# Performance work log

Hardware: AMD Instinct MI355X
Metric: run time of the kernel (lower is better)

## Reference

```python
import jax, jax.numpy as jnp
import numpy as np
import math

HIST = 10  # attention window over per-node prediction history


def setup_inputs() -> dict:
    key = jax.random.key(0)
    ks = jax.random.split(key, 16)
    N, DEG, F, H, M, O, P, S = 512, 8, 128, 256, 256, 64, 2, 64

    def lin(k, fan_in, shape):
        b = 1.0 / np.sqrt(fan_in)
        return jax.random.uniform(k, shape, jnp.float32, -b, b)

    return {
        "xa": jax.random.normal(ks[0], (N, F), jnp.float32),
        "neighbors": jax.random.randint(ks[1], (N, DEG), 0, N),
        "first_message": jax.random.normal(ks[2], (N, M), jnp.float32),
        "We": lin(ks[3], F, (F, H)), "be": lin(ks[3], F, (H,)),
        "Wq": lin(ks[4], M, (M, H)), "bq": lin(ks[4], M, (H,)),
        "Wk": lin(ks[5], H, (H, H)), "bk": lin(ks[5], H, (H,)),
        "Wr": lin(ks[6], 4 * H, (4 * H, H)), "br": lin(ks[6], 4 * H, (H,)),
        "Wm": lin(ks[7], H + M, (H + M, M)), "bm": lin(ks[7], H + M, (M,)),
        "Wd": lin(ks[8], H, (P, H, O)), "bd": lin(ks[8], H, (P, O)),
        "num_starts": S,
    }


def reference(xa, neighbors, first_message, We, be, Wq, bq, Wk, bk,
              Wr, br, Wm, bm, Wd, bd, num_starts):
    N, H = xa.shape[0], We.shape[1]
    M = first_message.shape[1]
    DEG = neighbors.shape[1]
    max_steps = 10 * N                    # message budget, as in the while-loop cap
    CAP = num_starts + max_steps * DEG    # static queue capacity bound
    inv_sqrt_h = 1.0 / math.sqrt(H)
    nbrs = neighbors.astype(jnp.int32)
    slot_ids = jnp.arange(HIST)

    encoded = xa @ We + be                                    # [N,H]
    hist = jnp.zeros((N, HIST, H), xa.dtype).at[:, 0, :].set(encoded)
    count = jnp.ones((N,), jnp.int32)
    q_node = jnp.zeros((CAP,), jnp.int32).at[:num_starts].set(
        jnp.arange(num_starts, dtype=jnp.int32))
    q_msg = jnp.zeros((CAP, M), xa.dtype).at[:num_starts].set(
        first_message[:num_starts])
    head = jnp.int32(0)
    tail = jnp.int32(num_starts)

    def step(carry, _):
        hist, count, q_node, q_msg, head, tail = carry
        active = head < tail                 # queue non-empty
        node = q_node[head]
        message = q_msg[head]                # [M]
        feats = hist[node]                   # [HIST,H] ring buffer of last states
        c = count[node]
        valid = slot_ids < jnp.minimum(c, HIST)
        # NOTE: source uses queries[0]/keys[0] for every head -> heads identical
        query = message @ Wq + bq            # [H]
        keys = feats @ Wk + bk               # [HIST,H]
        logits = jnp.where(valid, keys @ query * inv_sqrt_h, -jnp.inf)
        attn = jax.nn.softmax(logits)        # softmax over history axis (dim=-0)
        values = attn @ feats                # [H]
        newstate = jnp.concatenate([values] * 4) @ Wr + br     # [H]
        newmessage = jnp.concatenate([newstate, message]) @ Wm + bm  # [M]
        # conditional state updates (no-op writes when inactive)
        slot = c % HIST
        hist = hist.at[node, slot].set(jnp.where(active, newstate, hist[node, slot]))
        count = count.at[node].add(jnp.where(active, 1, 0))
        old_n = jax.lax.dynamic_slice(q_node, (tail,), (DEG,))
        old_m = jax.lax.dynamic_slice(q_msg, (tail, 0), (DEG, M))
        q_node = jax.lax.dynamic_update_slice(
            q_node, jnp.where(active, nbrs[node], old_n), (tail,))
        q_msg = jax.lax.dynamic_update_slice(
            q_msg, jnp.where(active, jnp.broadcast_to(newmessage, (DEG, M)), old_m),
            (tail, 0))
        head = head + jnp.where(active, 1, 0)
        tail = tail + jnp.where(active, DEG, 0)
        return (hist, count, q_node, q_msg, head, tail), None

    (hist, count, _, _, _, _), _ = jax.lax.scan(
        step, (hist, count, q_node, q_msg, head, tail), None, length=max_steps)

    final = hist[jnp.arange(N), (count - 1) % HIST]           # [N,H] last state
    logits = jnp.einsum('nh,pho->pno', final, Wd) + bd[:, None, :]
    return jax.nn.log_softmax(logits, axis=-1)                # [P,N,O]
```

## Files before the change

### kernel.cpp

```cpp
#include <hip/hip_runtime.h>
#include <hip/hip_bf16.h>

#define NN 512
#define DEG 8
#define FD 128
#define HD 256
#define MD 256
#define OD 64
#define PD 2
#define HIST 10
#define TOTAL (10 * NN)
#define NPAR 648
#define INV_SQRT_H 0.0625f

typedef __hip_bfloat16 bf16;

__device__ __forceinline__ float finz(float x) {
  unsigned u = __float_as_uint(x);
  return (((u >> 23) & 0xFFu) == 0xFFu) ? 0.f : x;
}

__device__ __forceinline__ float ldin(const void* p, int idx, int bf) {
  if (bf) return __bfloat162float(((const bf16*)p)[idx]);
  return ((const float*)p)[idx];
}

__device__ __forceinline__ float scload(const float* p) {
  return __uint_as_float(__hip_atomic_load((const unsigned*)p, __ATOMIC_RELAXED,
                                           __HIP_MEMORY_SCOPE_AGENT));
}
__device__ __forceinline__ void scstore(float* p, float v) {
  __hip_atomic_store((unsigned*)p, __float_as_uint(v), __ATOMIC_RELAXED,
                     __HIP_MEMORY_SCOPE_AGENT);
}

__device__ float g_hist[NN * HIST * HD];
__device__ float g_msgb[NPAR * MD];
__device__ float g_WQK[HD * HD];
__device__ float g_WrS[HD * HD];
__device__ float g_vq[HD];
__device__ float g_ck[HD];
__device__ float g_bqk;
__device__ int   g_node[TOTAL];
__device__ int   g_rank[TOTAL];
__device__ int   g_counts[NN];
__device__ int   g_off[NN];
__device__ int   g_list[TOTAL];
__device__ int   g_done[TOTAL];
__device__ int   g_dtype;
__device__ int   g_i64;

__device__ __forceinline__ int decode_S(const int* dS) {
  int r = dS[0];
  if (r >= 1 && r <= NN) return r;
  float f = __int_as_float(r);
  if (f >= 1.f && f <= (float)NN) return (int)f;
  unsigned u = ((unsigned)r & 0xFFFFu) << 16;
  float g = __uint_as_float(u);
  if (g >= 1.f && g <= (float)NN) return (int)g;
  return 64;
}

__device__ __forceinline__ int get_nbr(const int* nbrs, int i64, int n, int d) {
  int v = i64 ? nbrs[2 * (n * DEG + d)] : nbrs[n * DEG + d];
  return (v < 0) ? 0 : (v >= NN ? NN - 1 : v);
}

__global__ void __launch_bounds__(1024)
k_bfs(const unsigned* __restrict__ xa_w, const int* __restrict__ nbrs,
      const int* __restrict__ dS) {
  __shared__ int s_node[TOTAL];
  __shared__ int s_flags[1];
  const int t = threadIdx.x;
  if (t == 0) {
    int cnt = 0;
    for (int w = 0; w < 64; ++w) {
      unsigned lo = xa_w[w] & 0xFFFFu;
      float av = fabsf(__uint_as_float(lo << 16));
      if (av > 0.000244140625f && av < 64.f) ++cnt;
    }
    g_dtype = (cnt >= 32) ? 1 : 0;
    int allz = 1;
    for (int w = 1; w < 16; w += 2) allz &= (nbrs[w] == 0);
    g_i64 = allz;
    s_flags[0] = allz;
  }
  __syncthreads();
  const int i64 = s_flags[0];
  const int S = decode_S(dS);
  for (int i = t; i < S; i += 1024) s_node[i] = i;
  __syncthreads();
  int done = S;
  while (done < TOTAL) {
    long long nd = (long long)S + 8LL * (long long)done;
    int new_done = nd > (long long)TOTAL ? TOTAL : (int)nd;
    for (int i = done + t; i < new_done; i += 1024)
      s_node[i] = get_nbr(nbrs, i64, s_node[(i - S) >> 3], (i - S) & 7);
    __syncthreads();
    done = new_done;
  }
  for (int i = t; i < TOTAL; i += 1024) g_node[i] = s_node[i];
}

__global__ void __launch_bounds__(64)
k_rank() {
  const int n = blockIdx.x;
  const int l = threadIdx.x;
  if (l < HIST) g_done[n * HIST + l] = 0;
  int k = 0;
  for (int base = 0; base < TOTAL; base += 64) {
    int nd = g_node[base + l];
    unsigned long long m = __ballot(nd == n);
    if (nd == n) {
      unsigned long long below = m & ((1ull << l) - 1ull);
      g_rank[base + l] = k + (int)__popcll(below);
    }
    k += (int)__popcll(m);
  }
  if (l == 0) g_counts[n] = k;
}

__global__ void __launch_bounds__(1024)
k_csr() {
  __shared__ int s_sc[NN];
  const int t = threadIdx.x;
  if (t < NN) s_sc[t] = g_counts[t];
  __syncthreads();
  for (int d = 1; d < NN; d <<= 1) {
    int v = 0;
    if (t < NN && t >= d) v = s_sc[t - d];
    __syncthreads();
    if (t < NN) s_sc[t] += v;
    __syncthreads();
  }
  if (t < NN) g_off[t] = s_sc[t] - g_counts[t];
  __syncthreads();
  for (int e = t; e < TOTAL; e += 1024) {
    const int n = g_node[e];
    g_list[(s_sc[n] - g_counts[n]) + g_rank[e]] = e;
  }
}

__global__ void __launch_bounds__(1024)
k_weights(const void* __restrict__ xa, const void* __restrict__ We,
          const void* __restrict__ be, const void* __restrict__ Wq,
          const void* __restrict__ Wk, const void* __restrict__ Wr,
          const void* __restrict__ bq, const void* __restrict__ bk) {
  const int b = blockIdx.x, t = threadIdx.x;
  const int col = t & 255, grp = t >> 8;
  const int wave = t >> 6, lane = t & 63;
  const int bf = g_dtype;
  __shared__ float sw[HD];
  __shared__ float sp[4][HD];
  __shared__ float sr[16];
  if (b < HD) {
    if (grp == 0) sw[col] = ldin(Wq, b * HD + col, bf);
    __syncthreads();
    {
      const int h0 = grp * 64;
      float a0 = 0.f, a1 = 0.f, a2 = 0.f, a3 = 0.f;
      for (int h = 0; h < 64; h += 4) {
        a0 += sw[h0 + h]     * ldin(Wk, col * HD + h0 + h,     bf);
        a1 += sw[h0 + h + 1] * ldin(Wk, col * HD + h0 + h + 1, bf);
        a2 += sw[h0 + h + 2] * ldin(Wk, col * HD + h0 + h + 2, bf);
        a3 += sw[h0 + h + 3] * ldin(Wk, col * HD + h0 + h + 3, bf);
      }
      sp[grp][col] = (a0 + a1) + (a2 + a3);
    }
    if (grp == 1) {
      float pv = sw[col] * ldin(bk, col, bf);
#pragma unroll
      for (int off = 32; off > 0; off >>= 1) pv += __shfl_down(pv, off, 64);
      if (lane == 0) sr[wave] = pv;
    }
    if (grp == 2) {
      float s = 0.f;
#pragma unroll
      for (int q = 0; q < 4; ++q) s += ldin(Wr, (size_t)(q * HD + b) * HD + col, bf);
      g_WrS[b * HD + col] = s;
    }
    __syncthreads();
    if (grp == 0)
      g_WQK[b * HD + col] = (sp[0][col] + sp[1][col]) + (sp[2][col] + sp[3][col]);
    if (t == 0) g_vq[b] = (sr[4] + sr[5]) + (sr[6] + sr[7]);
  } else if (b == HD) {
    {
      const int h0 = grp * 64;
      float a0 = 0.f, a1 = 0.f, a2 = 0.f, a3 = 0.f;
      for (int h = 0; h < 64; h += 4) {
        a0 += ldin(Wk, col * HD + h0 + h,     bf) * ldin(bq, h0 + h,     bf);
        a1 += ldin(Wk, col * HD + h0 + h + 1, bf) * ldin(bq, h0 + h + 1, bf);
        a2 += ldin(Wk, col * HD + h0 + h + 2, bf) * ldin(bq, h0 + h + 2, bf);
        a3 += ldin(Wk, col * HD + h0 + h + 3, bf) * ldin(bq, h0 + h + 3, bf);
      }
      sp[grp][col] = (a0 + a1) + (a2 + a3);
    }
    if (grp == 1) {
      float pb = ldin(bq, col, bf) * ldin(bk, col, bf);
#pragma unroll
      for (int off = 32; off > 0; off >>= 1) pb += __shfl_down(pb, off, 64);
      if (lane == 0) sr[wave] = pb;
    }
    __syncthreads();
    if (grp == 0)
      g_ck[col] = (sp[0][col] + sp[1][col]) + (sp[2][col] + sp[3][col]);
    if (t == 0) g_bqk = (sr[4] + sr[5]) + (sr[6] + sr[7]);
  } else {
    const int n = b - HD - 1;
    if (t < FD) sw[t] = ldin(xa, n * FD + t, bf);
    __syncthreads();
    const int f0 = grp * 32;
    float a0 = 0.f, a1 = 0.f, a2 = 0.f, a3 = 0.f;
    for (int f = 0; f < 32; f += 4) {
      a0 += sw[f0 + f]     * ldin(We, (f0 + f)     * HD + col, bf);
      a1 += sw[f0 + f + 1] * ldin(We, (f0 + f + 1) * HD + col, bf);
      a2 += sw[f0 + f + 2] * ldin(We, (f0 + f + 2) * HD + col, bf);
      a3 += sw[f0 + f + 3] * ldin(We, (f0 + f + 3) * HD + col, bf);
    }
    sp[grp][col] = (a0 + a1) + (a2 + a3);
    __syncthreads();
    if (grp == 0)
      g_hist[(size_t)(n * HIST) * HD + col] =
          ldin(be, col, bf) + (sp[0][col] + sp[1][col]) + (sp[2][col] + sp[3][col]);
  }
}

__global__ void __launch_bounds__(256, 2)
k_flow(const void* __restrict__ fmsg, const void* __restrict__ br_,
       const void* __restrict__ Wm, const void* __restrict__ bm,
       const int* __restrict__ dS) {
  const int n = blockIdx.x;
  const int t = threadIdx.x;
  const int wave = t >> 6, lane = t & 63;
  const int S = decode_S(dS);
  const int bf = g_dtype;
  __shared__ float s_hist[HIST][HD];
  __shared__ float s_msg[MD];
  __shared__ float s_vals[HD];
  __shared__ float s_ns[HD];
  __shared__ float s_red[4][HIST + 1];
  const int cnt = g_counts[n];
  const int off = g_off[n];
#pragma unroll
  for (int j = 1; j < HIST; ++j) s_hist[j][t] = 0.f;
  s_hist[0][t] = finz(g_hist[(size_t)n * HIST * HD + t]);
  __syncthreads();

  for (int k = 0; k < cnt; ++k) {
    const int e = g_list[off + k];
    const int c = k + 1;
    const int v = (c < HIST) ? c : HIST;
    const int slot = c % HIST;
    const bool hc = (S + 8 * e) < TOTAL;

    float ms;
    if (e < S) {
      ms = ldin(fmsg, e * MD + t, bf);
    } else {
      const int p = (e - S) >> 3;
      if (t == 0)
        while (__hip_atomic_load(&g_done[p], __ATOMIC_RELAXED,
                                 __HIP_MEMORY_SCOPE_AGENT) == 0)
          __builtin_amdgcn_s_sleep(4);
      __syncthreads();
      ms = scload(g_msgb + (size_t)p * MD + t);
    }
    s_msg[t] = finz(ms);
    __syncthreads();

    float a0 = 0.f, a1 = 0.f, a2 = 0.f, a3 = 0.f;
    for (int m = 0; m < MD; m += 4) {
      a0 += s_msg[m]     * g_WQK[(m)     * HD + t];
      a1 += s_msg[m + 1] * g_WQK[(m + 1) * HD + t];
      a2 += s_msg[m + 2] * g_WQK[(m + 2) * HD + t];
      a3 += s_msg[m + 3] * g_WQK[(m + 3) * HD + t];
    }
    const float kq = g_ck[t] + ((a0 + a1) + (a2 + a3));

    float part[HIST + 1];
#pragma unroll
    for (int j = 0; j < HIST; ++j) part[j] = s_hist[j][t] * kq;
    part[HIST] = s_msg[t] * g_vq[t];
#pragma unroll
    for (int o = 32; o > 0; o >>= 1) {
#pragma unroll
      for (int j = 0; j <= HIST; ++j) part[j] += __shfl_down(part[j], o, 64);
    }
    if (lane == 0) {
#pragma unroll
      for (int j = 0; j <= HIST; ++j) s_red[wave][j] = part[j];
    }
    __syncthreads();

    float sc[HIST + 1];
#pragma unroll
    for (int j = 0; j <= HIST; ++j)
      sc[j] = (s_red[0][j] + s_red[1][j]) + (s_red[2][j] + s_red[3][j]);
    const float bkq = sc[HIST] + g_bqk;
    float lg[HIST];
#pragma unroll
    for (int j = 0; j < HIST; ++j)
      lg[j] = (j < v) ? ((sc[j] + bkq) * INV_SQRT_H) : -1e30f;
    float mx = lg[0];
#pragma unroll
    for (int j = 1; j < HIST; ++j) mx = fmaxf(mx, lg[j]);
    float e_[HIST], den = 0.f;
#pragma unroll
    for (int j = 0; j < HIST; ++j) { e_[j] = __expf(lg[j] - mx); den += e_[j]; }
    const float iden = 1.0f / den;
    float val = 0.f;
#pragma unroll
    for (int j = 0; j < HIST; ++j) val += e_[j] * s_hist[j][t];
    s_vals[t] = val * iden;
    __syncthreads();

    float b0 = 0.f, b1 = 0.f, b2 = 0.f, b3 = 0.f;
    for (int h = 0; h < HD; h += 4) {
      b0 += s_vals[h]     * g_WrS[(h)     * HD + t];
      b1 += s_vals[h + 1] * g_WrS[(h + 1) * HD + t];
      b2 += s_vals[h + 2] * g_WrS[(h + 2) * HD + t];
      b3 += s_vals[h + 3] * g_WrS[(h + 3) * HD + t];
    }
    const float ns = ldin(br_, t, bf) + ((b0 + b1) + (b2 + b3));
    s_hist[slot][t] = ns;
    if (k == cnt - 1)
      g_hist[(size_t)(n * HIST + slot) * HD + t] = ns;
    if (hc) s_ns[t] = ns;
    __syncthreads();

    if (hc) {
      float c0 = 0.f, c1 = 0.f, c2 = 0.f, c3 = 0.f;
      if (bf) {
        const bf16* w = (const bf16*)Wm;
        for (int h = 0; h < HD; h += 4) {
          c0 += s_ns[h]     * __bfloat162float(w[(h)     * MD + t]);
          c1 += s_ns[h + 1] * __bfloat162float(w[(h + 1) * MD + t]);
          c2 += s_ns[h + 2] * __bfloat162float(w[(h + 2) * MD + t]);
          c3 += s_ns[h + 3] * __bfloat162float(w[(h + 3) * MD + t]);
        }
        for (int m = 0; m < MD; m += 4) {
          c0 += s_msg[m]     * __bfloat162float(w[(HD + m)     * MD + t]);
          c1 += s_msg[m + 1] * __bfloat162float(w[(HD + m + 1) * MD + t]);
          c2 += s_msg[m + 2] * __bfloat162float(w[(HD + m + 2) * MD + t]);
          c3 += s_msg[m + 3] * __bfloat162float(w[(HD + m + 3) * MD + t]);
        }
      } else {
        const float* w = (const float*)Wm;
        for (int h = 0; h < HD; h += 4) {
          c0 += s_ns[h]     * w[(h)     * MD + t];
          c1 += s_ns[h + 1] * w[(h + 1) * MD + t];
          c2 += s_ns[h + 2] * w[(h + 2) * MD + t];
          c3 += s_ns[h + 3] * w[(h + 3) * MD + t];
        }
        for (int m = 0; m < MD; m += 4) {
          c0 += s_msg[m]     * w[(HD + m)     * MD + t];
          c1 += s_msg[m + 1] * w[(HD + m + 1) * MD + t];
          c2 += s_msg[m + 2] * w[(HD + m + 2) * MD + t];
          c3 += s_msg[m + 3] * w[(HD + m + 3) * MD + t];
        }
      }
      scstore(&g_msgb[(size_t)e * MD + t],
              ldin(bm, t, bf) + ((c0 + c1) + (c2 + c3)));
      asm volatile("s_waitcnt vmcnt(0)" ::: "memory");
    }
    __syncthreads();
    if (hc && t == 0)
      __hip_atomic_store(&g_done[e], 1, __ATOMIC_RELAXED,
                         __HIP_MEMORY_SCOPE_AGENT);
  }
}

__global__ void k_out(const void* __restrict__ Wd, const void* __restrict__ bd,
                      void* __restrict__ out) {
  __shared__ float sf[HD];
  const int b = blockIdx.x;
  const int pp = b >> 9;
  const int n = b & 511;
  const int t = threadIdx.x;
  const int bf = g_dtype;
  int occ = g_counts[n];
  if (occ < 0 || occ > TOTAL) occ = 0;
  const int slot = occ % HIST;
  for (int h = t; h < HD; h += OD) sf[h] = finz(g_hist[(size_t)(n * HIST + slot) * HD + h]);
  __syncthreads();
  float acc = finz(ldin(bd, pp * OD + t, bf));
  for (int h = 0; h < HD; ++h) acc += sf[h] * ldin(Wd, (pp * HD + h) * OD + t, bf);
  acc = finz(acc);
  float mx = acc;
#pragma unroll
  for (int off = 32; off > 0; off >>= 1) mx = fmaxf(mx, __shfl_xor(mx, off, 64));
  float ex = __expf(acc - mx);
  float s = ex;
#pragma unroll
  for (int off = 32; off > 0; off >>= 1) s += __shfl_xor(s, off, 64);
  float r = finz(acc - mx - logf(s));
  const int oi = (pp * NN + n) * OD + t;
  if (bf) ((bf16*)out)[oi] = __float2bfloat16(r);
  else    ((float*)out)[oi] = r;
}

extern "C" void kernel_launch(void* const* d_in, const int* in_sizes, int n_in,
                              void* d_out, int out_size, void* d_ws, size_t ws_size,
                              hipStream_t stream) {
  const void* xa   = d_in[0];
  const int*  nbrs = (const int*)d_in[1];
  const void* fmsg = d_in[2];
  const void* We   = d_in[3];
  const void* be   = d_in[4];
  const void* Wq   = d_in[5];
  const void* bq   = d_in[6];
  const void* Wk   = d_in[7];
  const void* bk   = d_in[8];
  const void* Wr   = d_in[9];
  const void* br   = d_in[10];
  const void* Wm   = d_in[11];
  const void* bm   = d_in[12];
  const void* Wd   = d_in[13];
  const void* bd   = d_in[14];
  const int*  dS   = (const int*)d_in[15];
  (void)d_ws; (void)ws_size; (void)in_sizes; (void)n_in; (void)out_size;

  k_bfs<<<dim3(1), dim3(1024), 0, stream>>>((const unsigned*)xa, nbrs, dS);
  k_rank<<<dim3(NN), dim3(64), 0, stream>>>();
  k_csr<<<dim3(1), dim3(1024), 0, stream>>>();
  k_weights<<<dim3(HD + 1 + NN), dim3(1024), 0, stream>>>(xa, We, be, Wq, Wk, Wr, bq, bk);
  k_flow<<<dim3(NN), dim3(256), 0, stream>>>(fmsg, br, Wm, bm, dS);
  k_out<<<dim3(PD * NN), dim3(OD), 0, stream>>>(Wd, bd, d_out);
}
```

Measured before the change: 482.4 us.

## Fuse prep kernels, build per-node lists in flow, and split matvecs across waves

Merges the BFS, rank, CSR and weight-precompute launches into one prep kernel. Each flow block now builds its own list of queue entries by scanning g_node in shared memory, so the global rank/CSR passes go away. The per-step matvecs (WQK, WrS, Wm) are split across the four waves by reduction dimension, with float4/ushort4 column loads and a shared-memory reduce. The attention score reduction now covers only three values per wave instead of eleven. In exchange each serial step gets more barriers, and the 20KB s_list plus the 20KB s_node array in the prep kernel raise shared-memory use, which may reduce occupancy.

```diff
diff --git a/kernel.cpp b/kernel.cpp
--- a/kernel.cpp
+++ b/kernel.cpp
@@ -25,6 +25,10 @@
   return ((const float*)p)[idx];
 }
 
+__device__ __forceinline__ float bfu(unsigned short u) {
+  return __uint_as_float(((unsigned)u) << 16);
+}
+
 __device__ __forceinline__ float scload(const float* p) {
   return __uint_as_float(__hip_atomic_load((const unsigned*)p, __ATOMIC_RELAXED,
                                            __HIP_MEMORY_SCOPE_AGENT));
@@ -42,10 +46,7 @@
 __device__ float g_ck[HD];
 __device__ float g_bqk;
 __device__ int   g_node[TOTAL];
-__device__ int   g_rank[TOTAL];
 __device__ int   g_counts[NN];
-__device__ int   g_off[NN];
-__device__ int   g_list[TOTAL];
 __device__ int   g_done[TOTAL];
 __device__ int   g_dtype;
 __device__ int   g_i64;
@@ -66,93 +67,30 @@
   return (v < 0) ? 0 : (v >= NN ? NN - 1 : v);
 }
 
+__device__ __forceinline__ int detect_bf(const unsigned* xa_w) {
+  const int lane = threadIdx.x & 63;
+  unsigned lo = xa_w[lane] & 0xFFFFu;
+  float av = fabsf(__uint_as_float(lo << 16));
+  unsigned long long m = __ballot(av > 0.000244140625f && av < 64.f);
+  return ((int)__popcll(m) >= 32) ? 1 : 0;
+}
+
 __global__ void __launch_bounds__(1024)
-k_bfs(const unsigned* __restrict__ xa_w, const int* __restrict__ nbrs,
-      const int* __restrict__ dS) {
-  __shared__ int s_node[TOTAL];
-  __shared__ int s_flags[1];
-  const int t = threadIdx.x;
-  if (t == 0) {
-    int cnt = 0;
-    for (int w = 0; w < 64; ++w) {
-      unsigned lo = xa_w[w] & 0xFFFFu;
-      float av = fabsf(__uint_as_float(lo << 16));
-      if (av > 0.000244140625f && av < 64.f) ++cnt;
-    }
-    g_dtype = (cnt >= 32) ? 1 : 0;
-    int allz = 1;
-    for (int w = 1; w < 16; w += 2) allz &= (nbrs[w] == 0);
-    g_i64 = allz;
-    s_flags[0] = allz;
-  }
-  __syncthreads();
-  const int i64 = s_flags[0];
-  const int S = decode_S(dS);
-  for (int i = t; i < S; i += 1024) s_node[i] = i;
-  __syncthreads();
-  int done = S;
-  while (done < TOTAL) {
-    long long nd = (long long)S + 8LL * (long long)done;
-    int new_done = nd > (long long)TOTAL ? TOTAL : (int)nd;
-    for (int i = done + t; i < new_done; i += 1024)
-      s_node[i] = get_nbr(nbrs, i64, s_node[(i - S) >> 3], (i - S) & 7);
-    __syncthreads();
-    done = new_done;
-  }
-  for (int i = t; i < TOTAL; i += 1024) g_node[i] = s_node[i];
-}
-
-__global__ void __launch_bounds__(64)
-k_rank() {
-  const int n = blockIdx.x;
-  const int l = threadIdx.x;
-  if (l < HIST) g_done[n * HIST + l] = 0;
-  int k = 0;
-  for (int base = 0; base < TOTAL; base += 64) {
-    int nd = g_node[base + l];
-    unsigned long long m = __ballot(nd == n);
-    if (nd == n) {
-      unsigned long long below = m & ((1ull << l) - 1ull);
-      g_rank[base + l] = k + (int)__popcll(below);
-    }
-    k += (int)__popcll(m);
-  }
-  if (l == 0) g_counts[n] = k;
-}
-
-__global__ void __launch_bounds__(1024)
-k_csr() {
-  __shared__ int s_sc[NN];
-  const int t = threadIdx.x;
-  if (t < NN) s_sc[t] = g_counts[t];
-  __syncthreads();
-  for (int d = 1; d < NN; d <<= 1) {
-    int v = 0;
-    if (t < NN && t >= d) v = s_sc[t - d];
-    __syncthreads();
-    if (t < NN) s_sc[t] += v;
-    __syncthreads();
-  }
-  if (t < NN) g_off[t] = s_sc[t] - g_counts[t];
-  __syncthreads();
-  for (int e = t; e < TOTAL; e += 1024) {
-    const int n = g_node[e];
-    g_list[(s_sc[n] - g_counts[n]) + g_rank[e]] = e;
-  }
-}
-
-__global__ void __launch_bounds__(1024)
-k_weights(const void* __restrict__ xa, const void* __restrict__ We,
-          const void* __restrict__ be, const void* __restrict__ Wq,
-          const void* __restrict__ Wk, const void* __restrict__ Wr,
-          const void* __restrict__ bq, const void* __restrict__ bk) {
+k_prep(const void* __restrict__ xa, const unsigned* __restrict__ xa_w,
+       const int* __restrict__ nbrs, const int* __restrict__ dS,
+       const void* __restrict__ We, const void* __restrict__ be,
+       const void* __restrict__ Wq, const void* __restrict__ Wk,
+       const void* __restrict__ Wr, const void* __restrict__ bq,
+       const void* __restrict__ bk) {
   const int b = blockIdx.x, t = threadIdx.x;
   const int col = t & 255, grp = t >> 8;
   const int wave = t >> 6, lane = t & 63;
-  const int bf = g_dtype;
+  const int bf = detect_bf(xa_w);
+  if (t < 8) { int fi = 8 * b + t; if (fi < TOTAL) g_done[fi] = 0; }
   __shared__ float sw[HD];
   __shared__ float sp[4][HD];
   __shared__ float sr[16];
+  __shared__ int s_node[TOTAL];
   if (b < HD) {
     if (grp == 0) sw[col] = ldin(Wq, b * HD + col, bf);
     __syncthreads();
@@ -205,7 +143,7 @@
     if (grp == 0)
       g_ck[col] = (sp[0][col] + sp[1][col]) + (sp[2][col] + sp[3][col]);
     if (t == 0) g_bqk = (sr[4] + sr[5]) + (sr[6] + sr[7]);
-  } else {
+  } else if (b <= HD + NN) {
     const int n = b - HD - 1;
     if (t < FD) sw[t] = ldin(xa, n * FD + t, bf);
     __syncthreads();
@@ -222,6 +160,25 @@
     if (grp == 0)
       g_hist[(size_t)(n * HIST) * HD + col] =
           ldin(be, col, bf) + (sp[0][col] + sp[1][col]) + (sp[2][col] + sp[3][col]);
+  } else {
+    if (t == 0) g_dtype = bf;
+    bool c8 = (lane < 8) ? (nbrs[2 * lane + 1] == 0) : true;
+    unsigned long long im = __ballot(c8);
+    const int i64 = ((im & 0xFFull) == 0xFFull) ? 1 : 0;
+    if (t == 0) g_i64 = i64;
+    const int S = decode_S(dS);
+    for (int i = t; i < S; i += 1024) s_node[i] = i;
+    __syncthreads();
+    int done = S;
+    while (done < TOTAL) {
+      long long nd = (long long)S + 8LL * (long long)done;
+      int new_done = nd > (long long)TOTAL ? TOTAL : (int)nd;
+      for (int i = done + t; i < new_done; i += 1024)
+        s_node[i] = get_nbr(nbrs, i64, s_node[(i - S) >> 3], (i - S) & 7);
+      __syncthreads();
+      done = new_done;
+    }
+    for (int i = t; i < TOTAL; i += 1024) g_node[i] = s_node[i];
   }
 }
 
@@ -232,71 +189,120 @@
   const int n = blockIdx.x;
   const int t = threadIdx.x;
   const int wave = t >> 6, lane = t & 63;
+  const int C = lane << 2;
   const int S = decode_S(dS);
   const int bf = g_dtype;
   __shared__ float s_hist[HIST][HD];
   __shared__ float s_msg[MD];
   __shared__ float s_vals[HD];
   __shared__ float s_ns[HD];
-  __shared__ float s_red[4][HIST + 1];
-  const int cnt = g_counts[n];
-  const int off = g_off[n];
+  __shared__ float s_p[4][HD];
+  __shared__ float s_red[4][3];
+  __shared__ int   s_list[TOTAL];
+  __shared__ int   s_cnt;
+
+  const float4 ck4 = *(const float4*)&g_ck[C];
+  const float4 vq4 = *(const float4*)&g_vq[C];
+  float4 br4, bm4;
+  br4.x = ldin(br_, C, bf);     br4.y = ldin(br_, C + 1, bf);
+  br4.z = ldin(br_, C + 2, bf); br4.w = ldin(br_, C + 3, bf);
+  bm4.x = ldin(bm, C, bf);      bm4.y = ldin(bm, C + 1, bf);
+  bm4.z = ldin(bm, C + 2, bf);  bm4.w = ldin(bm, C + 3, bf);
+  const float bqk = g_bqk;
+
 #pragma unroll
   for (int j = 1; j < HIST; ++j) s_hist[j][t] = 0.f;
   s_hist[0][t] = finz(g_hist[(size_t)n * HIST * HD + t]);
+
+  if (wave == 0) {
+    int k = 0;
+    for (int base = 0; base < TOTAL; base += 64) {
+      int nd = g_node[base + lane];
+      unsigned long long m = __ballot(nd == n);
+      if (nd == n) {
+        unsigned long long below = m & ((1ull << lane) - 1ull);
+        s_list[k + (int)__popcll(below)] = base + lane;
+      }
+      k += (int)__popcll(m);
+    }
+    if (lane == 0) { s_cnt = k; g_counts[n] = k; }
+  }
   __syncthreads();
+  const int cnt = s_cnt;
 
   for (int k = 0; k < cnt; ++k) {
-    const int e = g_list[off + k];
+    const int e = s_list[k];
     const int c = k + 1;
     const int v = (c < HIST) ? c : HIST;
     const int slot = c % HIST;
     const bool hc = (S + 8 * e) < TOTAL;
 
-    float ms;
     if (e < S) {
-      ms = ldin(fmsg, e * MD + t, bf);
+      s_msg[t] = finz(ldin(fmsg, e * MD + t, bf));
     } else {
       const int p = (e - S) >> 3;
       if (t == 0)
         while (__hip_atomic_load(&g_done[p], __ATOMIC_RELAXED,
                                  __HIP_MEMORY_SCOPE_AGENT) == 0)
-          __builtin_amdgcn_s_sleep(4);
+          __builtin_amdgcn_s_sleep(2);
       __syncthreads();
-      ms = scload(g_msgb + (size_t)p * MD + t);
-    }
-    s_msg[t] = finz(ms);
-    __syncthreads();
-
-    float a0 = 0.f, a1 = 0.f, a2 = 0.f, a3 = 0.f;
-    for (int m = 0; m < MD; m += 4) {
-      a0 += s_msg[m]     * g_WQK[(m)     * HD + t];
-      a1 += s_msg[m + 1] * g_WQK[(m + 1) * HD + t];
-      a2 += s_msg[m + 2] * g_WQK[(m + 2) * HD + t];
-      a3 += s_msg[m + 3] * g_WQK[(m + 3) * HD + t];
-    }
-    const float kq = g_ck[t] + ((a0 + a1) + (a2 + a3));
-
-    float part[HIST + 1];
-#pragma unroll
-    for (int j = 0; j < HIST; ++j) part[j] = s_hist[j][t] * kq;
-    part[HIST] = s_msg[t] * g_vq[t];
+      s_msg[t] = finz(scload(g_msgb + (size_t)p * MD + t));
+    }
+    __syncthreads();
+
+    {
+      const float* wp = g_WQK + (size_t)(64 * wave) * HD + C;
+      const float* mp = s_msg + 64 * wave;
+      float4 a0 = {0.f, 0.f, 0.f, 0.f}, a1 = {0.f, 0.f, 0.f, 0.f};
+      for (int m = 0; m < 64; m += 2) {
+        float s0 = mp[m], s1 = mp[m + 1];
+        float4 w0 = *(const float4*)(wp + (size_t)m * HD);
+        float4 w1 = *(const float4*)(wp + (size_t)(m + 1) * HD);
+        a0.x += s0 * w0.x; a0.y += s0 * w0.y; a0.z += s0 * w0.z; a0.w += s0 * w0.w;
+        a1.x += s1 * w1.x; a1.y += s1 * w1.y; a1.z += s1 * w1.z; a1.w += s1 * w1.w;
+      }
+      a0.x += a1.x; a0.y += a1.y; a0.z += a1.z; a0.w += a1.w;
+      *(float4*)&s_p[wave][C] = a0;
+    }
+    __syncthreads();
+    float4 kq4;
+    {
+      float4 q0 = *(const float4*)&s_p[0][C];
+      float4 q1 = *(const float4*)&s_p[1][C];
+      float4 q2 = *(const float4*)&s_p[2][C];
+      float4 q3 = *(const float4*)&s_p[3][C];
+      kq4.x = ck4.x + ((q0.x + q1.x) + (q2.x + q3.x));
+      kq4.y = ck4.y + ((q0.y + q1.y) + (q2.y + q3.y));
+      kq4.z = ck4.z + ((q0.z + q1.z) + (q2.z + q3.z));
+      kq4.w = ck4.w + ((q0.w + q1.w) + (q2.w + q3.w));
+    }
+
+    float4 h0 = *(const float4*)&s_hist[wave][C];
+    float4 h1 = *(const float4*)&s_hist[wave + 4][C];
+    float4 h2 = {0.f, 0.f, 0.f, 0.f};
+    float p0 = h0.x * kq4.x + h0.y * kq4.y + h0.z * kq4.z + h0.w * kq4.w;
+    float p1 = h1.x * kq4.x + h1.y * kq4.y + h1.z * kq4.z + h1.w * kq4.w;
+    float p2 = 0.f;
+    if (wave < 2) {
+      h2 = *(const float4*)&s_hist[wave + 8][C];
+      p2 = h2.x * kq4.x + h2.y * kq4.y + h2.z * kq4.z + h2.w * kq4.w;
+    } else if (wave == 2) {
+      float4 m4 = *(const float4*)&s_msg[C];
+      p2 = m4.x * vq4.x + m4.y * vq4.y + m4.z * vq4.z + m4.w * vq4.w;
+    }
 #pragma unroll
     for (int o = 32; o > 0; o >>= 1) {
-#pragma unroll
-      for (int j = 0; j <= HIST; ++j) part[j] += __shfl_down(part[j], o, 64);
-    }
-    if (lane == 0) {
-#pragma unroll
-      for (int j = 0; j <= HIST; ++j) s_red[wave][j] = part[j];
-    }
-    __syncthreads();
-
-    float sc[HIST + 1];
-#pragma unroll
-    for (int j = 0; j <= HIST; ++j)
-      sc[j] = (s_red[0][j] + s_red[1][j]) + (s_red[2][j] + s_red[3][j]);
-    const float bkq = sc[HIST] + g_bqk;
+      p0 += __shfl_down(p0, o, 64);
+      p1 += __shfl_down(p1, o, 64);
+      p2 += __shfl_down(p2, o, 64);
+    }
+    if (lane == 0) { s_red[wave][0] = p0; s_red[wave][1] = p1; s_red[wave][2] = p2; }
+    __syncthreads();
+
+    float sc[HIST];
+#pragma unroll
+    for (int j = 0; j < HIST; ++j) sc[j] = s_red[j & 3][j >> 2];
+    const float bkq = s_red[2][2] + bqk;
     float lg[HIST];
 #pragma unroll
     for (int j = 0; j < HIST; ++j)
@@ -308,65 +314,111 @@
 #pragma unroll
     for (int j = 0; j < HIST; ++j) { e_[j] = __expf(lg[j] - mx); den += e_[j]; }
     const float iden = 1.0f / den;
-    float val = 0.f;
-#pragma unroll
-    for (int j = 0; j < HIST; ++j) val += e_[j] * s_hist[j][t];
-    s_vals[t] = val * iden;
-    __syncthreads();
-
-    float b0 = 0.f, b1 = 0.f, b2 = 0.f, b3 = 0.f;
-    for (int h = 0; h < HD; h += 4) {
-      b0 += s_vals[h]     * g_WrS[(h)     * HD + t];
-      b1 += s_vals[h + 1] * g_WrS[(h + 1) * HD + t];
-      b2 += s_vals[h + 2] * g_WrS[(h + 2) * HD + t];
-      b3 += s_vals[h + 3] * g_WrS[(h + 3) * HD + t];
-    }
-    const float ns = ldin(br_, t, bf) + ((b0 + b1) + (b2 + b3));
-    s_hist[slot][t] = ns;
-    if (k == cnt - 1)
-      g_hist[(size_t)(n * HIST + slot) * HD + t] = ns;
-    if (hc) s_ns[t] = ns;
+
+    {
+      float4 vp;
+      vp.x = e_[wave] * h0.x + e_[wave + 4] * h1.x;
+      vp.y = e_[wave] * h0.y + e_[wave + 4] * h1.y;
+      vp.z = e_[wave] * h0.z + e_[wave + 4] * h1.z;
+      vp.w = e_[wave] * h0.w + e_[wave + 4] * h1.w;
+      if (wave < 2) {
+        vp.x += e_[wave + 8] * h2.x; vp.y += e_[wave + 8] * h2.y;
+        vp.z += e_[wave + 8] * h2.z; vp.w += e_[wave + 8] * h2.w;
+      }
+      *(float4*)&s_p[wave][C] = vp;
+    }
+    __syncthreads();
+    if (wave == 0) {
+      float4 q0 = *(const float4*)&s_p[0][C];
+      float4 q1 = *(const float4*)&s_p[1][C];
+      float4 q2 = *(const float4*)&s_p[2][C];
+      float4 q3 = *(const float4*)&s_p[3][C];
+      float4 v4;
+      v4.x = iden * ((q0.x + q1.x) + (q2.x + q3.x));
+      v4.y = iden * ((q0.y + q1.y) + (q2.y + q3.y));
+      v4.z = iden * ((q0.z + q1.z) + (q2.z + q3.z));
+      v4.w = iden * ((q0.w + q1.w) + (q2.w + q3.w));
+      *(float4*)&s_vals[C] = v4;
+    }
+    __syncthreads();
+
+    {
+      const float* wp = g_WrS + (size_t)(64 * wave) * HD + C;
+      const float* vp = s_vals + 64 * wave;
+      float4 a0 = {0.f, 0.f, 0.f, 0.f}, a1 = {0.f, 0.f, 0.f, 0.f};
+      for (int h = 0; h < 64; h += 2) {
+        float s0 = vp[h], s1 = vp[h + 1];
+        float4 w0 = *(const float4*)(wp + (size_t)h * HD);
+        float4 w1 = *(const float4*)(wp + (size_t)(h + 1) * HD);
+        a0.x += s0 * w0.x; a0.y += s0 * w0.y; a0.z += s0 * w0.z; a0.w += s0 * w0.w;
+        a1.x += s1 * w1.x; a1.y += s1 * w1.y; a1.z += s1 * w1.z; a1.w += s1 * w1.w;
+      }
+      a0.x += a1.x; a0.y += a1.y; a0.z += a1.z; a0.w += a1.w;
+      *(float4*)&s_p[wave][C] = a0;
+    }
+    __syncthreads();
+    if (wave == 0) {
+      float4 q0 = *(const float4*)&s_p[0][C];
+      float4 q1 = *(const float4*)&s_p[1][C];
+      float4 q2 = *(const float4*)&s_p[2][C];
+      float4 q3 = *(const float4*)&s_p[3][C];
+      float4 ns4;
+      ns4.x = br4.x + ((q0.x + q1.x) + (q2.x + q3.x));
+      ns4.y = br4.y + ((q0.y + q1.y) + (q2.y + q3.y));
+      ns4.z = br4.z + ((q0.z + q1.z) + (q2.z + q3.z));
+      ns4.w = br4.w + ((q0.w + q1.w) + (q2.w + q3.w));
+      *(float4*)&s_hist[slot][C] = ns4;
+      *(float4*)&s_ns[C] = ns4;
+      if (k == cnt - 1)
+        *(float4*)&g_hist[((size_t)(n * HIST + slot)) * HD + C] = ns4;
+    }
     __syncthreads();
 
     if (hc) {
-      float c0 = 0.f, c1 = 0.f, c2 = 0.f, c3 = 0.f;
+      const float* src = (wave < 2) ? (s_ns + 128 * wave) : (s_msg + 128 * (wave - 2));
+      float4 a0 = {0.f, 0.f, 0.f, 0.f}, a1 = {0.f, 0.f, 0.f, 0.f};
       if (bf) {
-        const bf16* w = (const bf16*)Wm;
-        for (int h = 0; h < HD; h += 4) {
-          c0 += s_ns[h]     * __bfloat162float(w[(h)     * MD + t]);
-          c1 += s_ns[h + 1] * __bfloat162float(w[(h + 1) * MD + t]);
-          c2 += s_ns[h + 2] * __bfloat162float(w[(h + 2) * MD + t]);
-          c3 += s_ns[h + 3] * __bfloat162float(w[(h + 3) * MD + t]);
-        }
-        for (int m = 0; m < MD; m += 4) {
-          c0 += s_msg[m]     * __bfloat162float(w[(HD + m)     * MD + t]);
-          c1 += s_msg[m + 1] * __bfloat162float(w[(HD + m + 1) * MD + t]);
-          c2 += s_msg[m + 2] * __bfloat162float(w[(HD + m + 2) * MD + t]);
-          c3 += s_msg[m + 3] * __bfloat162float(w[(HD + m + 3) * MD + t]);
+        const unsigned short* wb =
+            (const unsigned short*)Wm + (size_t)(128 * wave) * MD + C;
+        for (int r = 0; r < 128; r += 2) {
+          float s0 = src[r], s1 = src[r + 1];
+          ushort4 u0 = *(const ushort4*)(wb + (size_t)r * MD);
+          ushort4 u1 = *(const ushort4*)(wb + (size_t)(r + 1) * MD);
+          a0.x += s0 * bfu(u0.x); a0.y += s0 * bfu(u0.y);
+          a0.z += s0 * bfu(u0.z); a0.w += s0 * bfu(u0.w);
+          a1.x += s1 * bfu(u1.x); a1.y += s1 * bfu(u1.y);
+          a1.z += s1 * bfu(u1.z); a1.w += s1 * bfu(u1.w);
         }
       } else {
-        const float* w = (const float*)Wm;
-        for (int h = 0; h < HD; h += 4) {
-          c0 += s_ns[h]     * w[(h)     * MD + t];
-          c1 += s_ns[h + 1] * w[(h + 1) * MD + t];
-          c2 += s_ns[h + 2] * w[(h + 2) * MD + t];
-          c3 += s_ns[h + 3] * w[(h + 3) * MD + t];
+        const float* wf = (const float*)Wm + (size_t)(128 * wave) * MD + C;
+        for (int r = 0; r < 128; r += 2) {
+          float s0 = src[r], s1 = src[r + 1];
+          float4 w0 = *(const float4*)(wf + (size_t)r * MD);
+          float4 w1 = *(const float4*)(wf + (size_t)(r + 1) * MD);
+          a0.x += s0 * w0.x; a0.y += s0 * w0.y; a0.z += s0 * w0.z; a0.w += s0 * w0.w;
+          a1.x += s1 * w1.x; a1.y += s1 * w1.y; a1.z += s1 * w1.z; a1.w += s1 * w1.w;
         }
-        for (int m = 0; m < MD; m += 4) {
-          c0 += s_msg[m]     * w[(HD + m)     * MD + t];
-          c1 += s_msg[m + 1] * w[(HD + m + 1) * MD + t];
-          c2 += s_msg[m + 2] * w[(HD + m + 2) * MD + t];
-          c3 += s_msg[m + 3] * w[(HD + m + 3) * MD + t];
-        }
-      }
-      scstore(&g_msgb[(size_t)e * MD + t],
-              ldin(bm, t, bf) + ((c0 + c1) + (c2 + c3)));
-      asm volatile("s_waitcnt vmcnt(0)" ::: "memory");
-    }
-    __syncthreads();
-    if (hc && t == 0)
-      __hip_atomic_store(&g_done[e], 1, __ATOMIC_RELAXED,
-                         __HIP_MEMORY_SCOPE_AGENT);
+      }
+      a0.x += a1.x; a0.y += a1.y; a0.z += a1.z; a0.w += a1.w;
+      *(float4*)&s_p[wave][C] = a0;
+      __syncthreads();
+      if (wave == 0) {
+        float4 q0 = *(const float4*)&s_p[0][C];
+        float4 q1 = *(const float4*)&s_p[1][C];
+        float4 q2 = *(const float4*)&s_p[2][C];
+        float4 q3 = *(const float4*)&s_p[3][C];
+        float* dst = g_msgb + (size_t)e * MD + C;
+        scstore(dst,     bm4.x + ((q0.x + q1.x) + (q2.x + q3.x)));
+        scstore(dst + 1, bm4.y + ((q0.y + q1.y) + (q2.y + q3.y)));
+        scstore(dst + 2, bm4.z + ((q0.z + q1.z) + (q2.z + q3.z)));
+        scstore(dst + 3, bm4.w + ((q0.w + q1.w) + (q2.w + q3.w)));
+        asm volatile("s_waitcnt vmcnt(0)" ::: "memory");
+      }
+      __syncthreads();
+      if (t == 0)
+        __hip_atomic_store(&g_done[e], 1, __ATOMIC_RELAXED,
+                           __HIP_MEMORY_SCOPE_AGENT);
+    }
   }
 }
 
@@ -420,10 +472,8 @@
   const int*  dS   = (const int*)d_in[15];
   (void)d_ws; (void)ws_size; (void)in_sizes; (void)n_in; (void)out_size;
 
-  k_bfs<<<dim3(1), dim3(1024), 0, stream>>>((const unsigned*)xa, nbrs, dS);
-  k_rank<<<dim3(NN), dim3(64), 0, stream>>>();
-  k_csr<<<dim3(1), dim3(1024), 0, stream>>>();
-  k_weights<<<dim3(HD + 1 + NN), dim3(1024), 0, stream>>>(xa, We, be, Wq, Wk, Wr, bq, bk);
+  k_prep<<<dim3(HD + 1 + NN + 1), dim3(1024), 0, stream>>>(
+      xa, (const unsigned*)xa, nbrs, dS, We, be, Wq, Wk, Wr, bq, bk);
   k_flow<<<dim3(NN), dim3(256), 0, stream>>>(fmsg, br, Wm, bm, dS);
   k_out<<<dim3(PD * NN), dim3(OD), 0, stream>>>(Wd, bd, d_out);
 }
```

Measured after the change: 787.5 us. 63.2% more time.

## Fuse BFS and weight prep into one kernel; build per-node lists inside flow kernel

Applied to the files above, without the earlier changes.

Merges the BFS expansion, dtype/index-width detection and g_done reset into the weight-precompute kernel as an extra block. This removes three serial launches (k_bfs, k_rank, k_csr). Each flow block now scans g_node with one wave to build its own occurrence list in shared memory, which replaces the global rank/CSR arrays. The cost is 20KB of extra shared memory per block in k_prep and k_flow, which may lower occupancy. Every flow block also does a redundant 5120-entry scan before its serial loop.

```diff
diff --git a/kernel.cpp b/kernel.cpp
--- a/kernel.cpp
+++ b/kernel.cpp
@@ -42,10 +42,7 @@
 __device__ float g_ck[HD];
 __device__ float g_bqk;
 __device__ int   g_node[TOTAL];
-__device__ int   g_rank[TOTAL];
 __device__ int   g_counts[NN];
-__device__ int   g_off[NN];
-__device__ int   g_list[TOTAL];
 __device__ int   g_done[TOTAL];
 __device__ int   g_dtype;
 __device__ int   g_i64;
@@ -66,93 +63,30 @@
   return (v < 0) ? 0 : (v >= NN ? NN - 1 : v);
 }
 
+__device__ __forceinline__ int detect_bf(const unsigned* xa_w) {
+  const int lane = threadIdx.x & 63;
+  unsigned lo = xa_w[lane] & 0xFFFFu;
+  float av = fabsf(__uint_as_float(lo << 16));
+  unsigned long long m = __ballot(av > 0.000244140625f && av < 64.f);
+  return ((int)__popcll(m) >= 32) ? 1 : 0;
+}
+
 __global__ void __launch_bounds__(1024)
-k_bfs(const unsigned* __restrict__ xa_w, const int* __restrict__ nbrs,
-      const int* __restrict__ dS) {
-  __shared__ int s_node[TOTAL];
-  __shared__ int s_flags[1];
-  const int t = threadIdx.x;
-  if (t == 0) {
-    int cnt = 0;
-    for (int w = 0; w < 64; ++w) {
-      unsigned lo = xa_w[w] & 0xFFFFu;
-      float av = fabsf(__uint_as_float(lo << 16));
-      if (av > 0.000244140625f && av < 64.f) ++cnt;
-    }
-    g_dtype = (cnt >= 32) ? 1 : 0;
-    int allz = 1;
-    for (int w = 1; w < 16; w += 2) allz &= (nbrs[w] == 0);
-    g_i64 = allz;
-    s_flags[0] = allz;
-  }
-  __syncthreads();
-  const int i64 = s_flags[0];
-  const int S = decode_S(dS);
-  for (int i = t; i < S; i += 1024) s_node[i] = i;
-  __syncthreads();
-  int done = S;
-  while (done < TOTAL) {
-    long long nd = (long long)S + 8LL * (long long)done;
-    int new_done = nd > (long long)TOTAL ? TOTAL : (int)nd;
-    for (int i = done + t; i < new_done; i += 1024)
-      s_node[i] = get_nbr(nbrs, i64, s_node[(i - S) >> 3], (i - S) & 7);
-    __syncthreads();
-    done = new_done;
-  }
-  for (int i = t; i < TOTAL; i += 1024) g_node[i] = s_node[i];
-}
-
-__global__ void __launch_bounds__(64)
-k_rank() {
-  const int n = blockIdx.x;
-  const int l = threadIdx.x;
-  if (l < HIST) g_done[n * HIST + l] = 0;
-  int k = 0;
-  for (int base = 0; base < TOTAL; base += 64) {
-    int nd = g_node[base + l];
-    unsigned long long m = __ballot(nd == n);
-    if (nd == n) {
-      unsigned long long below = m & ((1ull << l) - 1ull);
-      g_rank[base + l] = k + (int)__popcll(below);
-    }
-    k += (int)__popcll(m);
-  }
-  if (l == 0) g_counts[n] = k;
-}
-
-__global__ void __launch_bounds__(1024)
-k_csr() {
-  __shared__ int s_sc[NN];
-  const int t = threadIdx.x;
-  if (t < NN) s_sc[t] = g_counts[t];
-  __syncthreads();
-  for (int d = 1; d < NN; d <<= 1) {
-    int v = 0;
-    if (t < NN && t >= d) v = s_sc[t - d];
-    __syncthreads();
-    if (t < NN) s_sc[t] += v;
-    __syncthreads();
-  }
-  if (t < NN) g_off[t] = s_sc[t] - g_counts[t];
-  __syncthreads();
-  for (int e = t; e < TOTAL; e += 1024) {
-    const int n = g_node[e];
-    g_list[(s_sc[n] - g_counts[n]) + g_rank[e]] = e;
-  }
-}
-
-__global__ void __launch_bounds__(1024)
-k_weights(const void* __restrict__ xa, const void* __restrict__ We,
-          const void* __restrict__ be, const void* __restrict__ Wq,
-          const void* __restrict__ Wk, const void* __restrict__ Wr,
-          const void* __restrict__ bq, const void* __restrict__ bk) {
+k_prep(const void* __restrict__ xa, const unsigned* __restrict__ xa_w,
+       const int* __restrict__ nbrs, const int* __restrict__ dS,
+       const void* __restrict__ We, const void* __restrict__ be,
+       const void* __restrict__ Wq, const void* __restrict__ Wk,
+       const void* __restrict__ Wr, const void* __restrict__ bq,
+       const void* __restrict__ bk) {
   const int b = blockIdx.x, t = threadIdx.x;
   const int col = t & 255, grp = t >> 8;
   const int wave = t >> 6, lane = t & 63;
-  const int bf = g_dtype;
+  const int bf = detect_bf(xa_w);
+  if (t < 8) { int fi = 8 * b + t; if (fi < TOTAL) g_done[fi] = 0; }
   __shared__ float sw[HD];
   __shared__ float sp[4][HD];
   __shared__ float sr[16];
+  __shared__ int s_node[TOTAL];
   if (b < HD) {
     if (grp == 0) sw[col] = ldin(Wq, b * HD + col, bf);
     __syncthreads();
@@ -205,7 +139,7 @@
     if (grp == 0)
       g_ck[col] = (sp[0][col] + sp[1][col]) + (sp[2][col] + sp[3][col]);
     if (t == 0) g_bqk = (sr[4] + sr[5]) + (sr[6] + sr[7]);
-  } else {
+  } else if (b <= HD + NN) {
     const int n = b - HD - 1;
     if (t < FD) sw[t] = ldin(xa, n * FD + t, bf);
     __syncthreads();
@@ -222,6 +156,25 @@
     if (grp == 0)
       g_hist[(size_t)(n * HIST) * HD + col] =
           ldin(be, col, bf) + (sp[0][col] + sp[1][col]) + (sp[2][col] + sp[3][col]);
+  } else {
+    if (t == 0) g_dtype = bf;
+    bool c8 = (lane < 8) ? (nbrs[2 * lane + 1] == 0) : true;
+    unsigned long long im = __ballot(c8);
+    const int i64 = ((im & 0xFFull) == 0xFFull) ? 1 : 0;
+    if (t == 0) g_i64 = i64;
+    const int S = decode_S(dS);
+    for (int i = t; i < S; i += 1024) s_node[i] = i;
+    __syncthreads();
+    int done = S;
+    while (done < TOTAL) {
+      long long nd = (long long)S + 8LL * (long long)done;
+      int new_done = nd > (long long)TOTAL ? TOTAL : (int)nd;
+      for (int i = done + t; i < new_done; i += 1024)
+        s_node[i] = get_nbr(nbrs, i64, s_node[(i - S) >> 3], (i - S) & 7);
+      __syncthreads();
+      done = new_done;
+    }
+    for (int i = t; i < TOTAL; i += 1024) g_node[i] = s_node[i];
   }
 }
 
@@ -239,15 +192,31 @@
   __shared__ float s_vals[HD];
   __shared__ float s_ns[HD];
   __shared__ float s_red[4][HIST + 1];
-  const int cnt = g_counts[n];
-  const int off = g_off[n];
+  __shared__ int   s_list[TOTAL];
+  __shared__ int   s_cnt;
+
 #pragma unroll
   for (int j = 1; j < HIST; ++j) s_hist[j][t] = 0.f;
   s_hist[0][t] = finz(g_hist[(size_t)n * HIST * HD + t]);
+
+  if (wave == 0) {
+    int k = 0;
+    for (int base = 0; base < TOTAL; base += 64) {
+      int nd = g_node[base + lane];
+      unsigned long long m = __ballot(nd == n);
+      if (nd == n) {
+        unsigned long long below = m & ((1ull << lane) - 1ull);
+        s_list[k + (int)__popcll(below)] = base + lane;
+      }
+      k += (int)__popcll(m);
+    }
+    if (lane == 0) { s_cnt = k; g_counts[n] = k; }
+  }
   __syncthreads();
+  const int cnt = s_cnt;
 
   for (int k = 0; k < cnt; ++k) {
-    const int e = g_list[off + k];
+    const int e = s_list[k];
     const int c = k + 1;
     const int v = (c < HIST) ? c : HIST;
     const int slot = c % HIST;
@@ -420,10 +389,8 @@
   const int*  dS   = (const int*)d_in[15];
   (void)d_ws; (void)ws_size; (void)in_sizes; (void)n_in; (void)out_size;
 
-  k_bfs<<<dim3(1), dim3(1024), 0, stream>>>((const unsigned*)xa, nbrs, dS);
-  k_rank<<<dim3(NN), dim3(64), 0, stream>>>();
-  k_csr<<<dim3(1), dim3(1024), 0, stream>>>();
-  k_weights<<<dim3(HD + 1 + NN), dim3(1024), 0, stream>>>(xa, We, be, Wq, Wk, Wr, bq, bk);
+  k_prep<<<dim3(HD + 1 + NN + 1), dim3(1024), 0, stream>>>(
+      xa, (const unsigned*)xa, nbrs, dS, We, be, Wq, Wk, Wr, bq, bk);
   k_flow<<<dim3(NN), dim3(256), 0, stream>>>(fmsg, br, Wm, bm, dS);
   k_out<<<dim3(PD * NN), dim3(OD), 0, stream>>>(Wd, bd, d_out);
 }
```

Measured after the change: 465.7 us. 3.5% less time.
